# Kernel optimization log

Measured on AMD Instinct MI355X. Metric: run time of the kernel, lower is better.

## Reference

```python
import jax, jax.numpy as jnp
import numpy as np

HIDDEN = 128
POOL = 64
G = 4            # grid_size
NBHD = 2.0       # neighborhood_size (meters)
NUM_SCENES = 256
PEDS = 64        # pedestrians per scene (uniform seq_start_end)


def setup_inputs() -> dict:
    key = jax.random.key(0)
    k1, k2, k3 = jax.random.split(key, 3)
    hidden_states = jax.random.normal(k1, (NUM_SCENES * PEDS, HIDDEN), jnp.float32)
    positions = jax.random.uniform(k2, (NUM_SCENES * PEDS, 2), jnp.float32)
    fan_in = HIDDEN * G * G
    weight = jax.random.normal(k3, (fan_in, POOL), jnp.float32) / np.sqrt(fan_in)
    bias = jnp.zeros((POOL,), jnp.float32)
    return {
        "hidden_states": hidden_states,
        "positions": positions,
        "weight": weight,
        "bias": bias,
        "peds_per_scene": PEDS,
    }


def reference(hidden_states, positions, weight, bias, peds_per_scene):
    total, H = hidden_states.shape
    P = peds_per_scene
    B = total // P
    h = hidden_states.reshape(B, P, H)
    p = positions.reshape(B, P, 2)

    # rel[b, i, j] = pos[j] - pos[i]  (matches curr_pos - curr_pos[i:i+1])
    rel = p[:, None, :, :] - p[:, :, None, :]            # [B, P, P, 2]
    in_range = (jnp.abs(rel[..., 0]) <= NBHD) & (jnp.abs(rel[..., 1]) <= NBHD)
    not_self = ~jnp.eye(P, dtype=bool)[None]
    mask = in_range & not_self                            # [B, P, P]

    # int() truncation == floor here since (rel + NBHD) >= 0 inside the range check
    scale = G / (2.0 * NBHD)
    gx = jnp.clip(jnp.floor((rel[..., 0] + NBHD) * scale).astype(jnp.int32), 0, G - 1)
    gy = jnp.clip(jnp.floor((rel[..., 1] + NBHD) * scale).astype(jnp.int32), 0, G - 1)
    grid_idx = gy * G + gx                                # [B, P, P]

    # scatter-add of neighbor hidden states into G*G bins via masked one-hot
    onehot = jax.nn.one_hot(grid_idx, G * G, dtype=h.dtype) * mask[..., None].astype(h.dtype)
    grid = jnp.einsum('bijg,bjh->bigh', onehot, h)        # [B, P, G*G, H]

    flat = grid.reshape(B * P, G * G * H)                 # row-major: (grid_idx, hidden)
    return flat @ weight + bias                            # [total_peds, POOL]
```

## Files before the change

kernel.cpp:

```cpp
#include <hip/hip_runtime.h>
#include <cstdint>

#define PEDS   64
#define HIDDEN 128
#define POOL   64
#define GRIDG  4
#define NBHD   2.0f

typedef unsigned short u16;
typedef unsigned int   u32;
typedef __attribute__((ext_vector_type(8))) short bf16x8;
typedef __attribute__((ext_vector_type(4))) float f32x4;

__device__ __forceinline__ u16 f2bf(float f) {
    u32 u = __float_as_uint(f);
    u += 0x7fffu + ((u >> 16) & 1u);
    return (u16)(u >> 16);
}
__device__ __forceinline__ u32 pack2bf(float a, float b) {
    return (u32)f2bf(a) | ((u32)f2bf(b) << 16);
}

__global__ __launch_bounds__(512) void social_fused(
    const float* __restrict__ h, const float* __restrict__ pos,
    const float* __restrict__ w, const float* __restrict__ bias,
    float* __restrict__ out)
{
    __shared__ unsigned char LB[65536];
    unsigned char* gidx  = LB;
    u32*           wmask = (u32*)(LB + 4096);
    u16*           hA    = (u16*)(LB + 8192);
    u16*           hwT   = (u16*)(LB + 57344);

    const int s    = blockIdx.x;
    const int tid  = threadIdx.x;
    const int wv   = tid >> 6;
    const int lane = tid & 63;
    const int l15  = lane & 15;
    const int q    = lane >> 4;
    const int mt   = wv & 3;
    const int nh   = wv >> 2;

    float2 pp = ((const float2*)pos)[(size_t)s * PEDS + lane];
    float px = pp.x, py = pp.y;

    const int hrow = tid >> 3, hc = tid & 7;
    const float4* hsrc = (const float4*)(h + ((size_t)s * PEDS + hrow) * HIDDEN + hc * 16);
    float4 hv0 = hsrc[0], hv1 = hsrc[1], hv2 = hsrc[2], hv3 = hsrc[3];

    const int gi  = wv * 8 + (lane >> 3);
    const int gj0 = (lane & 7) * 8;
    const float pxi = __shfl(px, gi), pyi = __shfl(py, gi);
    u32 gpk0 = 0, gpk1 = 0, um = 0;
    const float scale = (float)GRIDG / (2.0f * NBHD);
#pragma unroll
    for (int u8 = 0; u8 < 8; ++u8) {
        int j = gj0 + u8;
        float rx = __shfl(px, j) - pxi;
        float ry = __shfl(py, j) - pyi;
        u32 gb = 0xffu;
        if ((gi != j) && (fabsf(rx) <= NBHD) && (fabsf(ry) <= NBHD)) {
            int gx = (int)floorf((rx + NBHD) * scale); gx = min(max(gx, 0), GRIDG - 1);
            int gy = (int)floorf((ry + NBHD) * scale); gy = min(max(gy, 0), GRIDG - 1);
            int g = gy * GRIDG + gx;
            gb = (u32)g; um |= 1u << g;
        }
        if (u8 < 4) gpk0 |= gb << (u8 * 8); else gpk1 |= gb << ((u8 - 4) * 8);
    }
    *(uint2*)&gidx[gi * 64 + gj0] = make_uint2(gpk0, gpk1);

#pragma unroll
    for (int off = 32; off; off >>= 1) um |= __shfl_xor(um, off);
    if (lane == 0) wmask[wv] = um;

    {
        u32 p0 = pack2bf(hv0.x, hv0.y), p1 = pack2bf(hv0.z, hv0.w);
        u32 p2 = pack2bf(hv1.x, hv1.y), p3 = pack2bf(hv1.z, hv1.w);
        int ch = hc * 2;
        *(uint4*)&hA[hrow * 128 + ((ch ^ (hrow & 15)) << 3)] = make_uint4(p0, p1, p2, p3);
        p0 = pack2bf(hv2.x, hv2.y); p1 = pack2bf(hv2.z, hv2.w);
        p2 = pack2bf(hv3.x, hv3.y); p3 = pack2bf(hv3.z, hv3.w);
        ch = hc * 2 + 1;
        *(uint4*)&hA[hrow * 128 + ((ch ^ (hrow & 15)) << 3)] = make_uint4(p0, p1, p2, p3);
    }
    __syncthreads();

    u32 mask = wmask[0] | wmask[1] | wmask[2] | wmask[3]
             | wmask[4] | wmask[5] | wmask[6] | wmask[7];
    mask = __builtin_amdgcn_readfirstlane(mask);

    bf16x8 af[4];
#pragma unroll
    for (int st4 = 0; st4 < 4; ++st4)
        af[st4] = *(const bf16x8*)&hA[(mt * 16 + l15) * 128 + (((st4 * 4 + q) ^ l15) << 3)];

    const int ng = __popc(mask);
    u32 rem = mask;
    int g = 0;
    if (rem) { g = __ffs(rem) - 1; rem &= rem - 1u; }

    float wr[16];
    const int wc = lane, wk = wv * 16;
    if (ng) {
        const float* wsrc = w + ((size_t)g * HIDDEN + wk) * POOL + wc;
#pragma unroll
        for (int e = 0; e < 16; ++e) wr[e] = wsrc[(size_t)e * POOL];
    }

    f32x4 oacc[2];
    oacc[0] = (f32x4){0.f, 0.f, 0.f, 0.f};
    oacc[1] = (f32x4){0.f, 0.f, 0.f, 0.f};

    for (int t = 0; t < ng; ++t) {
        u16* wSb = (u16*)(LB + 24576 + ((t & 1) << 14));
#pragma unroll
        for (int cc = 0; cc < 2; ++cc) {
            u32 p0 = pack2bf(wr[cc * 8 + 0], wr[cc * 8 + 1]);
            u32 p1 = pack2bf(wr[cc * 8 + 2], wr[cc * 8 + 3]);
            u32 p2 = pack2bf(wr[cc * 8 + 4], wr[cc * 8 + 5]);
            u32 p3 = pack2bf(wr[cc * 8 + 6], wr[cc * 8 + 7]);
            int ch = wv * 2 + cc;
            *(uint4*)&wSb[wc * 128 + ((ch ^ (wc & 15)) << 3)] = make_uint4(p0, p1, p2, p3);
        }
        int gn = -1;
        if (rem) { gn = __ffs(rem) - 1; rem &= rem - 1u; }
        if (gn >= 0) {
            const float* wsrc = w + ((size_t)gn * HIDDEN + wk) * POOL + wc;
#pragma unroll
            for (int e = 0; e < 16; ++e) wr[e] = wsrc[(size_t)e * POOL];
        }
        __syncthreads();

        f32x4 a1[2];
        a1[0] = (f32x4){0.f, 0.f, 0.f, 0.f};
        a1[1] = (f32x4){0.f, 0.f, 0.f, 0.f};
#pragma unroll
        for (int st4 = 0; st4 < 4; ++st4) {
            int chs = ((st4 * 4 + q) ^ l15) << 3;
            bf16x8 b0 = *(const bf16x8*)&wSb[(nh * 32 + l15) * 128 + chs];
            bf16x8 b1 = *(const bf16x8*)&wSb[(nh * 32 + 16 + l15) * 128 + chs];
            a1[0] = __builtin_amdgcn_mfma_f32_16x16x32_bf16(af[st4], b0, a1[0], 0, 0, 0);
            a1[1] = __builtin_amdgcn_mfma_f32_16x16x32_bf16(af[st4], b1, a1[1], 0, 0, 0);
        }
#pragma unroll
        for (int ni = 0; ni < 2; ++ni) {
            int c = nh * 32 + ni * 16 + l15;
            u32 lo = pack2bf(a1[ni][0], a1[ni][1]);
            u32 hi = pack2bf(a1[ni][2], a1[ni][3]);
            *(uint2*)&hwT[c * 64 + (((mt * 4 + q) ^ (c & 15)) << 2)] = make_uint2(lo, hi);
        }
        __syncthreads();

#pragma unroll
        for (int kk = 0; kk < 2; ++kk) {
            uint2 gg = *(const uint2*)&gidx[(mt * 16 + l15) * 64 + kk * 32 + q * 8];
            union { u16 hx[8]; bf16x8 v; } mu;
#pragma unroll
            for (int b = 0; b < 4; ++b)
                mu.hx[b]     = (((gg.x >> (b * 8)) & 0xffu) == (u32)g) ? (u16)0x3F80 : (u16)0;
#pragma unroll
            for (int b = 0; b < 4; ++b)
                mu.hx[4 + b] = (((gg.y >> (b * 8)) & 0xffu) == (u32)g) ? (u16)0x3F80 : (u16)0;
#pragma unroll
            for (int ni = 0; ni < 2; ++ni) {
                int c = nh * 32 + ni * 16 + l15;
                int cs = c & 15;
                uint2 b0 = *(const uint2*)&hwT[c * 64 + (((kk * 8 + q * 2 + 0) ^ cs) << 2)];
                uint2 b1 = *(const uint2*)&hwT[c * 64 + (((kk * 8 + q * 2 + 1) ^ cs) << 2)];
                union { u32 u[4]; bf16x8 v; } bu;
                bu.u[0] = b0.x; bu.u[1] = b0.y; bu.u[2] = b1.x; bu.u[3] = b1.y;
                oacc[ni] = __builtin_amdgcn_mfma_f32_16x16x32_bf16(mu.v, bu.v, oacc[ni], 0, 0, 0);
            }
        }
        g = gn;
    }

#pragma unroll
    for (int ni = 0; ni < 2; ++ni) {
        int c = nh * 32 + ni * 16 + l15;
        float bv = bias[c];
        size_t ob = ((size_t)s * PEDS + mt * 16 + q * 4) * POOL + c;
#pragma unroll
        for (int r = 0; r < 4; ++r)
            out[ob + (size_t)r * POOL] = oacc[ni][r] + bv;
    }
}

extern "C" void kernel_launch(void* const* d_in, const int* in_sizes, int n_in,
                              void* d_out, int out_size, void* d_ws, size_t ws_size,
                              hipStream_t stream) {
    const float* h    = (const float*)d_in[0];
    const float* pos  = (const float*)d_in[1];
    const float* w    = (const float*)d_in[2];
    const float* bias = (const float*)d_in[3];
    float* out = (float*)d_out;

    const int total = in_sizes[0] / HIDDEN;
    const int B     = total / PEDS;

    hipLaunchKernelGGL(social_fused, dim3(B), dim3(512), 0, stream,
                       h, pos, w, bias, out);
}
```

Before: 70.98 us.

## Split each scene across two 256-thread blocks by output column half

Each scene is now handled by two blocks of 256 threads, each computing 32 of the 64 pooled output columns, instead of one 512-thread block doing all 64. Shared memory per block drops from 64KB to 44KB, allowing two blocks per CU and twice as many blocks in the grid. In exchange, both blocks redundantly load hidden states, build the bf16 copy, and compute the neighbor grid indices for the same scene.

```diff
diff --git a/kernel.cpp b/kernel.cpp
--- a/kernel.cpp
+++ b/kernel.cpp
@@ -21,40 +21,43 @@
     return (u32)f2bf(a) | ((u32)f2bf(b) << 16);
 }
 
-__global__ __launch_bounds__(512) void social_fused(
+__global__ __launch_bounds__(256, 2) void social_fused(
     const float* __restrict__ h, const float* __restrict__ pos,
     const float* __restrict__ w, const float* __restrict__ bias,
     float* __restrict__ out)
 {
-    __shared__ unsigned char LB[65536];
+    __shared__ unsigned char LB[45056];
     unsigned char* gidx  = LB;
     u32*           wmask = (u32*)(LB + 4096);
     u16*           hA    = (u16*)(LB + 8192);
-    u16*           hwT   = (u16*)(LB + 57344);
-
-    const int s    = blockIdx.x;
+    u16*           hwT   = (u16*)(LB + 40960);
+
+    const int s    = blockIdx.x >> 1;
+    const int nh   = blockIdx.x & 1;
     const int tid  = threadIdx.x;
     const int wv   = tid >> 6;
     const int lane = tid & 63;
     const int l15  = lane & 15;
     const int q    = lane >> 4;
-    const int mt   = wv & 3;
-    const int nh   = wv >> 2;
+    const int mt   = wv;
 
     float2 pp = ((const float2*)pos)[(size_t)s * PEDS + lane];
     float px = pp.x, py = pp.y;
 
-    const int hrow = tid >> 3, hc = tid & 7;
-    const float4* hsrc = (const float4*)(h + ((size_t)s * PEDS + hrow) * HIDDEN + hc * 16);
-    float4 hv0 = hsrc[0], hv1 = hsrc[1], hv2 = hsrc[2], hv3 = hsrc[3];
-
-    const int gi  = wv * 8 + (lane >> 3);
-    const int gj0 = (lane & 7) * 8;
+    const int hrow = tid >> 2, hc = tid & 3;
+    const float4* hsrc = (const float4*)(h + ((size_t)s * PEDS + hrow) * HIDDEN + hc * 32);
+    float4 hv[8];
+#pragma unroll
+    for (int i = 0; i < 8; ++i) hv[i] = hsrc[i];
+
+    const int gi  = wv * 16 + (lane >> 2);
+    const int gj0 = (lane & 3) * 16;
     const float pxi = __shfl(px, gi), pyi = __shfl(py, gi);
-    u32 gpk0 = 0, gpk1 = 0, um = 0;
+    u32 gpk[4] = {0u, 0u, 0u, 0u};
+    u32 um = 0;
     const float scale = (float)GRIDG / (2.0f * NBHD);
 #pragma unroll
-    for (int u8 = 0; u8 < 8; ++u8) {
+    for (int u8 = 0; u8 < 16; ++u8) {
         int j = gj0 + u8;
         float rx = __shfl(px, j) - pxi;
         float ry = __shfl(py, j) - pyi;
@@ -65,28 +68,26 @@
             int g = gy * GRIDG + gx;
             gb = (u32)g; um |= 1u << g;
         }
-        if (u8 < 4) gpk0 |= gb << (u8 * 8); else gpk1 |= gb << ((u8 - 4) * 8);
-    }
-    *(uint2*)&gidx[gi * 64 + gj0] = make_uint2(gpk0, gpk1);
+        gpk[u8 >> 2] |= gb << ((u8 & 3) * 8);
+    }
+    *(uint4*)&gidx[gi * 64 + gj0] = make_uint4(gpk[0], gpk[1], gpk[2], gpk[3]);
 
 #pragma unroll
     for (int off = 32; off; off >>= 1) um |= __shfl_xor(um, off);
     if (lane == 0) wmask[wv] = um;
 
-    {
-        u32 p0 = pack2bf(hv0.x, hv0.y), p1 = pack2bf(hv0.z, hv0.w);
-        u32 p2 = pack2bf(hv1.x, hv1.y), p3 = pack2bf(hv1.z, hv1.w);
-        int ch = hc * 2;
+#pragma unroll
+    for (int k2 = 0; k2 < 4; ++k2) {
+        u32 p0 = pack2bf(hv[2 * k2].x, hv[2 * k2].y);
+        u32 p1 = pack2bf(hv[2 * k2].z, hv[2 * k2].w);
+        u32 p2 = pack2bf(hv[2 * k2 + 1].x, hv[2 * k2 + 1].y);
+        u32 p3 = pack2bf(hv[2 * k2 + 1].z, hv[2 * k2 + 1].w);
+        int ch = hc * 4 + k2;
         *(uint4*)&hA[hrow * 128 + ((ch ^ (hrow & 15)) << 3)] = make_uint4(p0, p1, p2, p3);
-        p0 = pack2bf(hv2.x, hv2.y); p1 = pack2bf(hv2.z, hv2.w);
-        p2 = pack2bf(hv3.x, hv3.y); p3 = pack2bf(hv3.z, hv3.w);
-        ch = hc * 2 + 1;
-        *(uint4*)&hA[hrow * 128 + ((ch ^ (hrow & 15)) << 3)] = make_uint4(p0, p1, p2, p3);
     }
     __syncthreads();
 
-    u32 mask = wmask[0] | wmask[1] | wmask[2] | wmask[3]
-             | wmask[4] | wmask[5] | wmask[6] | wmask[7];
+    u32 mask = wmask[0] | wmask[1] | wmask[2] | wmask[3];
     mask = __builtin_amdgcn_readfirstlane(mask);
 
     bf16x8 af[4];
@@ -100,9 +101,10 @@
     if (rem) { g = __ffs(rem) - 1; rem &= rem - 1u; }
 
     float wr[16];
-    const int wc = lane, wk = wv * 16;
+    const int wc = lane & 31;
+    const int wk = wv * 32 + (lane >> 5) * 16;
     if (ng) {
-        const float* wsrc = w + ((size_t)g * HIDDEN + wk) * POOL + wc;
+        const float* wsrc = w + ((size_t)g * HIDDEN + wk) * POOL + nh * 32 + wc;
 #pragma unroll
         for (int e = 0; e < 16; ++e) wr[e] = wsrc[(size_t)e * POOL];
     }
@@ -112,20 +114,20 @@
     oacc[1] = (f32x4){0.f, 0.f, 0.f, 0.f};
 
     for (int t = 0; t < ng; ++t) {
-        u16* wSb = (u16*)(LB + 24576 + ((t & 1) << 14));
+        u16* wSb = (u16*)(LB + 24576 + ((t & 1) << 13));
 #pragma unroll
         for (int cc = 0; cc < 2; ++cc) {
             u32 p0 = pack2bf(wr[cc * 8 + 0], wr[cc * 8 + 1]);
             u32 p1 = pack2bf(wr[cc * 8 + 2], wr[cc * 8 + 3]);
             u32 p2 = pack2bf(wr[cc * 8 + 4], wr[cc * 8 + 5]);
             u32 p3 = pack2bf(wr[cc * 8 + 6], wr[cc * 8 + 7]);
-            int ch = wv * 2 + cc;
+            int ch = (wk >> 3) + cc;
             *(uint4*)&wSb[wc * 128 + ((ch ^ (wc & 15)) << 3)] = make_uint4(p0, p1, p2, p3);
         }
         int gn = -1;
         if (rem) { gn = __ffs(rem) - 1; rem &= rem - 1u; }
         if (gn >= 0) {
-            const float* wsrc = w + ((size_t)gn * HIDDEN + wk) * POOL + wc;
+            const float* wsrc = w + ((size_t)gn * HIDDEN + wk) * POOL + nh * 32 + wc;
 #pragma unroll
             for (int e = 0; e < 16; ++e) wr[e] = wsrc[(size_t)e * POOL];
         }
@@ -137,14 +139,14 @@
 #pragma unroll
         for (int st4 = 0; st4 < 4; ++st4) {
             int chs = ((st4 * 4 + q) ^ l15) << 3;
-            bf16x8 b0 = *(const bf16x8*)&wSb[(nh * 32 + l15) * 128 + chs];
-            bf16x8 b1 = *(const bf16x8*)&wSb[(nh * 32 + 16 + l15) * 128 + chs];
+            bf16x8 b0 = *(const bf16x8*)&wSb[(l15) * 128 + chs];
+            bf16x8 b1 = *(const bf16x8*)&wSb[(16 + l15) * 128 + chs];
             a1[0] = __builtin_amdgcn_mfma_f32_16x16x32_bf16(af[st4], b0, a1[0], 0, 0, 0);
             a1[1] = __builtin_amdgcn_mfma_f32_16x16x32_bf16(af[st4], b1, a1[1], 0, 0, 0);
         }
 #pragma unroll
         for (int ni = 0; ni < 2; ++ni) {
-            int c = nh * 32 + ni * 16 + l15;
+            int c = ni * 16 + l15;
             u32 lo = pack2bf(a1[ni][0], a1[ni][1]);
             u32 hi = pack2bf(a1[ni][2], a1[ni][3]);
             *(uint2*)&hwT[c * 64 + (((mt * 4 + q) ^ (c & 15)) << 2)] = make_uint2(lo, hi);
@@ -163,7 +165,7 @@
                 mu.hx[4 + b] = (((gg.y >> (b * 8)) & 0xffu) == (u32)g) ? (u16)0x3F80 : (u16)0;
 #pragma unroll
             for (int ni = 0; ni < 2; ++ni) {
-                int c = nh * 32 + ni * 16 + l15;
+                int c = ni * 16 + l15;
                 int cs = c & 15;
                 uint2 b0 = *(const uint2*)&hwT[c * 64 + (((kk * 8 + q * 2 + 0) ^ cs) << 2)];
                 uint2 b1 = *(const uint2*)&hwT[c * 64 + (((kk * 8 + q * 2 + 1) ^ cs) << 2)];
@@ -198,6 +200,6 @@
     const int total = in_sizes[0] / HIDDEN;
     const int B     = total / PEDS;
 
-    hipLaunchKernelGGL(social_fused, dim3(B), dim3(512), 0, stream,
+    hipLaunchKernelGGL(social_fused, dim3(B * 2), dim3(256), 0, stream,
                        h, pos, w, bias, out);
 }
```

Result: slower. 74.28 us (+4.6%).

## Batch four grid cells per iteration to cut barriers and expose load parallelism

Applied to the files above, without the earlier changes.

The per-cell loop (one weight slice staged, GEMM1, GEMM2 per occupied grid cell, two barriers each) becomes a loop over groups of up to four cells. All four weight slices are loaded and staged into shared memory before one barrier, the four GEMM1 results are written to a larger hwT buffer, and GEMM2 runs over all of them after a second barrier. This cuts the barrier count by about four and lets more global loads be in flight at once, but drops the register prefetch that overlapped the next weight load with compute. LDS use grows to about 104 KB per block and register pressure rises, which can reduce occupancy.

```diff
diff --git a/kernel.cpp b/kernel.cpp
--- a/kernel.cpp
+++ b/kernel.cpp
@@ -26,11 +26,12 @@
     const float* __restrict__ w, const float* __restrict__ bias,
     float* __restrict__ out)
 {
-    __shared__ unsigned char LB[65536];
+    __shared__ unsigned char LB[106496];
     unsigned char* gidx  = LB;
     u32*           wmask = (u32*)(LB + 4096);
     u16*           hA    = (u16*)(LB + 8192);
-    u16*           hwT   = (u16*)(LB + 57344);
+    u16*           hwT   = (u16*)(LB + 8192);
+    u16*           wS    = (u16*)(LB + 40960);
 
     const int s    = blockIdx.x;
     const int tid  = threadIdx.x;
@@ -94,85 +95,89 @@
     for (int st4 = 0; st4 < 4; ++st4)
         af[st4] = *(const bf16x8*)&hA[(mt * 16 + l15) * 128 + (((st4 * 4 + q) ^ l15) << 3)];
 
-    const int ng = __popc(mask);
-    u32 rem = mask;
-    int g = 0;
-    if (rem) { g = __ffs(rem) - 1; rem &= rem - 1u; }
-
-    float wr[16];
-    const int wc = lane, wk = wv * 16;
-    if (ng) {
-        const float* wsrc = w + ((size_t)g * HIDDEN + wk) * POOL + wc;
-#pragma unroll
-        for (int e = 0; e < 16; ++e) wr[e] = wsrc[(size_t)e * POOL];
-    }
-
     f32x4 oacc[2];
     oacc[0] = (f32x4){0.f, 0.f, 0.f, 0.f};
     oacc[1] = (f32x4){0.f, 0.f, 0.f, 0.f};
 
-    for (int t = 0; t < ng; ++t) {
-        u16* wSb = (u16*)(LB + 24576 + ((t & 1) << 14));
-#pragma unroll
-        for (int cc = 0; cc < 2; ++cc) {
-            u32 p0 = pack2bf(wr[cc * 8 + 0], wr[cc * 8 + 1]);
-            u32 p1 = pack2bf(wr[cc * 8 + 2], wr[cc * 8 + 3]);
-            u32 p2 = pack2bf(wr[cc * 8 + 4], wr[cc * 8 + 5]);
-            u32 p3 = pack2bf(wr[cc * 8 + 6], wr[cc * 8 + 7]);
-            int ch = wv * 2 + cc;
-            *(uint4*)&wSb[wc * 128 + ((ch ^ (wc & 15)) << 3)] = make_uint4(p0, p1, p2, p3);
-        }
-        int gn = -1;
-        if (rem) { gn = __ffs(rem) - 1; rem &= rem - 1u; }
-        if (gn >= 0) {
-            const float* wsrc = w + ((size_t)gn * HIDDEN + wk) * POOL + wc;
-#pragma unroll
-            for (int e = 0; e < 16; ++e) wr[e] = wsrc[(size_t)e * POOL];
-        }
+    u32 rem = mask;
+    const int wc = lane, wk = wv * 16;
+
+    while (rem) {
+        int cg0, cg1 = -1, cg2 = -1, cg3 = -1;
+        cg0 = __ffs(rem) - 1; rem &= rem - 1u;
+        if (rem) { cg1 = __ffs(rem) - 1; rem &= rem - 1u;
+            if (rem) { cg2 = __ffs(rem) - 1; rem &= rem - 1u;
+                if (rem) { cg3 = __ffs(rem) - 1; rem &= rem - 1u; } } }
+
+#define STAGE_CELL(T, CG) if ((CG) >= 0) { \
+        const float* wsrc = w + ((size_t)(CG) * HIDDEN + wk) * POOL + wc; \
+        float wr[16]; \
+        _Pragma("unroll") for (int e = 0; e < 16; ++e) wr[e] = wsrc[(size_t)e * POOL]; \
+        u16* wSb = wS + (T) * 8192; \
+        _Pragma("unroll") for (int cc = 0; cc < 2; ++cc) { \
+            u32 p0 = pack2bf(wr[cc*8+0], wr[cc*8+1]); \
+            u32 p1 = pack2bf(wr[cc*8+2], wr[cc*8+3]); \
+            u32 p2 = pack2bf(wr[cc*8+4], wr[cc*8+5]); \
+            u32 p3 = pack2bf(wr[cc*8+6], wr[cc*8+7]); \
+            int ch = wv * 2 + cc; \
+            *(uint4*)&wSb[wc * 128 + ((ch ^ (wc & 15)) << 3)] = make_uint4(p0, p1, p2, p3); \
+        } }
+
+        STAGE_CELL(0, cg0)
+        STAGE_CELL(1, cg1)
+        STAGE_CELL(2, cg2)
+        STAGE_CELL(3, cg3)
+
         __syncthreads();
 
-        f32x4 a1[2];
-        a1[0] = (f32x4){0.f, 0.f, 0.f, 0.f};
-        a1[1] = (f32x4){0.f, 0.f, 0.f, 0.f};
-#pragma unroll
-        for (int st4 = 0; st4 < 4; ++st4) {
-            int chs = ((st4 * 4 + q) ^ l15) << 3;
-            bf16x8 b0 = *(const bf16x8*)&wSb[(nh * 32 + l15) * 128 + chs];
-            bf16x8 b1 = *(const bf16x8*)&wSb[(nh * 32 + 16 + l15) * 128 + chs];
-            a1[0] = __builtin_amdgcn_mfma_f32_16x16x32_bf16(af[st4], b0, a1[0], 0, 0, 0);
-            a1[1] = __builtin_amdgcn_mfma_f32_16x16x32_bf16(af[st4], b1, a1[1], 0, 0, 0);
-        }
-#pragma unroll
-        for (int ni = 0; ni < 2; ++ni) {
-            int c = nh * 32 + ni * 16 + l15;
-            u32 lo = pack2bf(a1[ni][0], a1[ni][1]);
-            u32 hi = pack2bf(a1[ni][2], a1[ni][3]);
-            *(uint2*)&hwT[c * 64 + (((mt * 4 + q) ^ (c & 15)) << 2)] = make_uint2(lo, hi);
-        }
+#define GEMM1_CELL(T, CG) if ((CG) >= 0) { \
+        const u16* wSb = wS + (T) * 8192; \
+        f32x4 a10 = (f32x4){0.f,0.f,0.f,0.f}, a11 = (f32x4){0.f,0.f,0.f,0.f}; \
+        _Pragma("unroll") for (int st4 = 0; st4 < 4; ++st4) { \
+            int chs = ((st4 * 4 + q) ^ l15) << 3; \
+            bf16x8 b0 = *(const bf16x8*)&wSb[(nh * 32 + l15) * 128 + chs]; \
+            bf16x8 b1 = *(const bf16x8*)&wSb[(nh * 32 + 16 + l15) * 128 + chs]; \
+            a10 = __builtin_amdgcn_mfma_f32_16x16x32_bf16(af[st4], b0, a10, 0, 0, 0); \
+            a11 = __builtin_amdgcn_mfma_f32_16x16x32_bf16(af[st4], b1, a11, 0, 0, 0); \
+        } \
+        { int c = nh * 32 + l15; int cs = c & 15; \
+          *(uint2*)&hwT[c * 256 + (T) * 64 + (((mt * 4 + q) ^ cs) << 2)] = \
+              make_uint2(pack2bf(a10[0], a10[1]), pack2bf(a10[2], a10[3])); } \
+        { int c = nh * 32 + 16 + l15; int cs = c & 15; \
+          *(uint2*)&hwT[c * 256 + (T) * 64 + (((mt * 4 + q) ^ cs) << 2)] = \
+              make_uint2(pack2bf(a11[0], a11[1]), pack2bf(a11[2], a11[3])); } }
+
+        GEMM1_CELL(0, cg0)
+        GEMM1_CELL(1, cg1)
+        GEMM1_CELL(2, cg2)
+        GEMM1_CELL(3, cg3)
+
         __syncthreads();
 
 #pragma unroll
         for (int kk = 0; kk < 2; ++kk) {
             uint2 gg = *(const uint2*)&gidx[(mt * 16 + l15) * 64 + kk * 32 + q * 8];
-            union { u16 hx[8]; bf16x8 v; } mu;
-#pragma unroll
-            for (int b = 0; b < 4; ++b)
-                mu.hx[b]     = (((gg.x >> (b * 8)) & 0xffu) == (u32)g) ? (u16)0x3F80 : (u16)0;
-#pragma unroll
-            for (int b = 0; b < 4; ++b)
-                mu.hx[4 + b] = (((gg.y >> (b * 8)) & 0xffu) == (u32)g) ? (u16)0x3F80 : (u16)0;
-#pragma unroll
-            for (int ni = 0; ni < 2; ++ni) {
-                int c = nh * 32 + ni * 16 + l15;
-                int cs = c & 15;
-                uint2 b0 = *(const uint2*)&hwT[c * 64 + (((kk * 8 + q * 2 + 0) ^ cs) << 2)];
-                uint2 b1 = *(const uint2*)&hwT[c * 64 + (((kk * 8 + q * 2 + 1) ^ cs) << 2)];
-                union { u32 u[4]; bf16x8 v; } bu;
-                bu.u[0] = b0.x; bu.u[1] = b0.y; bu.u[2] = b1.x; bu.u[3] = b1.y;
-                oacc[ni] = __builtin_amdgcn_mfma_f32_16x16x32_bf16(mu.v, bu.v, oacc[ni], 0, 0, 0);
-            }
+
+#define GEMM2_CELL(T, CG) if ((CG) >= 0) { \
+            union { u16 hx[8]; bf16x8 v; } mu; \
+            _Pragma("unroll") for (int b = 0; b < 4; ++b) \
+                mu.hx[b]     = (((gg.x >> (b * 8)) & 0xffu) == (u32)(CG)) ? (u16)0x3F80 : (u16)0; \
+            _Pragma("unroll") for (int b = 0; b < 4; ++b) \
+                mu.hx[4 + b] = (((gg.y >> (b * 8)) & 0xffu) == (u32)(CG)) ? (u16)0x3F80 : (u16)0; \
+            _Pragma("unroll") for (int ni = 0; ni < 2; ++ni) { \
+                int c = nh * 32 + ni * 16 + l15; int cs = c & 15; \
+                uint2 b0 = *(const uint2*)&hwT[c * 256 + (T) * 64 + (((kk * 8 + q * 2 + 0) ^ cs) << 2)]; \
+                uint2 b1 = *(const uint2*)&hwT[c * 256 + (T) * 64 + (((kk * 8 + q * 2 + 1) ^ cs) << 2)]; \
+                union { u32 u[4]; bf16x8 v; } bu; \
+                bu.u[0] = b0.x; bu.u[1] = b0.y; bu.u[2] = b1.x; bu.u[3] = b1.y; \
+                oacc[ni] = __builtin_amdgcn_mfma_f32_16x16x32_bf16(mu.v, bu.v, oacc[ni], 0, 0, 0); \
+            } }
+
+            GEMM2_CELL(0, cg0)
+            GEMM2_CELL(1, cg1)
+            GEMM2_CELL(2, cg2)
+            GEMM2_CELL(3, cg3)
         }
-        g = gn;
     }
 
 #pragma unroll
```

New measurement: 71.12 us. Within noise of the previous version (+0.2%).
